# Performance work log

Hardware: AMD Instinct MI355X
Metric: run time of the kernel (lower is better)

## Reference

```python
import jax, jax.numpy as jnp
import numpy as np

B, N, D, K = 4, 4096, 64, 16
SCALE = float(np.sqrt(D))


def setup_inputs() -> dict:
    key = jax.random.key(0)
    ks = jax.random.split(key, 16)
    f = lambda i, shape: jax.random.normal(ks[i], shape, dtype=jnp.float32) * 0.05
    return {
        'x': jax.random.normal(ks[0], (B, N, D), dtype=jnp.float32),
        'pos': jax.random.uniform(ks[1], (B, N, 3), dtype=jnp.float32),
        'Wq': f(2, (D, D)), 'Wk': f(3, (D, D)), 'Wv': f(4, (D, D)),
        'P1': f(5, (3, D)), 'p1b': f(6, (D,)), 'P2': f(7, (D, D)), 'p2b': f(8, (D,)),
        'A1': f(9, (D, D)), 'a1b': f(10, (D,)), 'A2': f(11, (D, D)), 'a2b': f(12, (D,)),
        'Wf': f(13, (D, D)), 'bf': f(14, (D,)),
    }


def _gather(feats, idx):
    # feats: [B,N,C], idx: [B,N,K] -> [B,N,K,C]  (index_points / idx_pt)
    return jax.vmap(lambda f, i: f[i])(feats, idx)


def reference(x, pos, Wq, Wk, Wv, P1, p1b, P2, p2b, A1, a1b, A2, a2b, Wf, bf):
    # kNN via squared distances (same math as square_distance + argsort[:, :, :k])
    sq = jnp.sum(pos * pos, axis=-1)                                   # [B,N]
    dists = sq[:, :, None] + sq[:, None, :] - 2.0 * jnp.einsum('bnc,bmc->bnm', pos, pos)
    _, idx = jax.lax.top_k(-dists, K)                                  # [B,N,K]

    knn_xyz = _gather(pos, idx)                                        # [B,N,K,3]
    q = x @ Wq                                                         # [B,N,D]
    kf = _gather(x @ Wk, idx)                                          # [B,N,K,D]
    v = _gather(x @ Wv, idx)                                           # [B,N,K,D]

    rel = pos[:, :, None, :] - knn_xyz                                 # [B,N,K,3]
    pos_enc = jax.nn.relu(rel @ P1 + p1b) @ P2 + p2b                   # [B,N,K,D]

    attn = jax.nn.relu((q[:, :, None, :] - kf + pos_enc) @ A1 + a1b) @ A2 + a2b
    attn = jax.nn.softmax(attn / SCALE, axis=-2)                       # softmax over K

    agg = jnp.sum(attn * (v + pos_enc), axis=2)                        # [B,N,D]
    return agg @ Wf + bf + x                                           # residual
```

## Files before the change

kernel.cpp:

```cpp
#include <hip/hip_runtime.h>
#include <hip/hip_bf16.h>
#include <stdint.h>

#define B_ 4
#define N_ 4096
#define D_ 64
#define K_ 16

static const size_t OFS_WQA1  = 0;
static const size_t OFS_WKA1  = 4096;
static const size_t OFS_WCOMB = 8192;
static const size_t OFS_C1    = 16384;
static const size_t OFS_QA1   = 16448;
static const size_t OFS_KA1   = OFS_QA1 + (size_t)B_*N_*64;
static const size_t OFS_V     = OFS_KA1 + (size_t)B_*N_*64;
static const size_t OFS_IDX   = OFS_V   + (size_t)B_*N_*64;
static const size_t OFS_POS4  = OFS_IDX + (size_t)B_*N_*16;
static const size_t OFS_BF16  = OFS_POS4 + (size_t)B_*N_*4;
static const size_t OFS_PBF   = OFS_BF16 + 6144;
static const size_t OFS_WFB   = OFS_PBF + 6144;
static const size_t OFS_APK   = OFS_WFB + 2048;
static const size_t OFS_BPK   = OFS_APK + 262144;

#define KNN_CAP 96

typedef __attribute__((ext_vector_type(8))) short short8;
typedef __attribute__((ext_vector_type(4))) float floatx4;

__device__ __forceinline__ unsigned short f2bf(float f) {
    __hip_bfloat16 h = __float2bfloat16(f);
    return *reinterpret_cast<unsigned short*>(&h);
}

__device__ __forceinline__ float bf2f(unsigned short u) {
    __hip_bfloat16 h = *reinterpret_cast<__hip_bfloat16*>(&u);
    return __bfloat162float(h);
}

__device__ __forceinline__ unsigned long long bsortu64(unsigned long long v, int l) {
#pragma unroll
    for (int k = 2; k <= 64; k <<= 1) {
#pragma unroll
        for (int j = k >> 1; j > 0; j >>= 1) {
            unsigned long long o = __shfl_xor(v, j, 64);
            unsigned long long mn = v < o ? v : o;
            unsigned long long mx = v < o ? o : v;
            v = ((((l & j) == 0) == ((l & k) == 0))) ? mn : mx;
        }
    }
    return v;
}

__device__ __forceinline__ void bsortu64x2(unsigned long long& a, unsigned long long& b, int l) {
#pragma unroll
    for (int k = 2; k <= 64; k <<= 1) {
#pragma unroll
        for (int j = k >> 1; j > 0; j >>= 1) {
            unsigned long long oa = __shfl_xor(a, j, 64);
            unsigned long long ob = __shfl_xor(b, j, 64);
            bool up = (((l & j) == 0) == ((l & k) == 0));
            unsigned long long mna = a < oa ? a : oa, mxa = a < oa ? oa : a;
            unsigned long long mnb = b < ob ? b : ob, mxb = b < ob ? ob : b;
            a = up ? mna : mxa;
            b = up ? mnb : mxb;
        }
    }
}

__global__ __launch_bounds__(256) void k_pre(
        const float* __restrict__ Wq, const float* __restrict__ Wk,
        const float* __restrict__ Wv, const float* __restrict__ Wf,
        const float* __restrict__ P2, const float* __restrict__ A1,
        const float* __restrict__ p2b, const float* __restrict__ a1b,
        const float* __restrict__ pos, float* __restrict__ ws) {
    int blk = blockIdx.x;
    unsigned short* pbf = (unsigned short*)(ws + OFS_PBF);
    if (blk < 65) {
        int i = blk * 256 + threadIdx.x;
        if (i < 4096) {
            int c = i >> 6, d = i & 63;
            float s = 0.f;
            for (int e = 0; e < 64; ++e) s = fmaf(Wq[c*64+e], A1[e*64+d], s);
            ws[OFS_WQA1 + i] = s;
            pbf[d*64 + c] = f2bf(s);
        } else if (i < 8192) {
            int j = i - 4096; int c = j >> 6, d = j & 63;
            float s = 0.f;
            for (int e = 0; e < 64; ++e) s = fmaf(Wk[c*64+e], A1[e*64+d], s);
            ws[OFS_WKA1 + j] = s;
            pbf[(64+d)*64 + c] = f2bf(s);
        } else if (i < 16384) {
            int j = i - 8192; int c = j >> 7, dd = j & 127;
            float s;
            if (dd < 64) { s = 0.f; for (int e = 0; e < 64; ++e) s = fmaf(P2[c*64+e], A1[e*64+dd], s); }
            else s = P2[c*64 + (dd - 64)];
            ws[OFS_WCOMB + j] = s;
        } else if (i < 16448) {
            int d = i - 16384;
            float s = a1b[d];
            for (int e = 0; e < 64; ++e) s = fmaf(p2b[e], A1[e*64+d], s);
            ws[OFS_C1 + d] = s;
        }
    } else if (blk < 81) {
        int i = (blk - 65) * 256 + threadIdx.x;
        int c = i >> 6, d = i & 63;
        pbf[(128+d)*64 + c] = f2bf(Wv[c*64+d]);
    } else if (blk < 97) {
        int i = (blk - 81) * 256 + threadIdx.x;
        int c = i >> 6, d = i & 63;
        ((unsigned short*)(ws + OFS_WFB))[d*64 + c] = f2bf(Wf[c*64+d]);
    } else {
        int i = (blk - 97) * 256 + threadIdx.x;
        float px = pos[(size_t)i*3+0], py = pos[(size_t)i*3+1], pz = pos[(size_t)i*3+2];
        float sq = fmaf(pz, pz, fmaf(py, py, px*px));
        ((float4*)(ws + OFS_POS4))[i] = make_float4(px, py, pz, sq);

        unsigned short xh = f2bf(px), yh = f2bf(py), zh = f2bf(pz), sh = f2bf(sq);
        float xl = px - bf2f(xh), yl = py - bf2f(yh), zl = pz - bf2f(zh), sl = sq - bf2f(sh);
        unsigned short xlb = f2bf(xl), ylb = f2bf(yl), zlb = f2bf(zl), slb = f2bf(sl);
        unsigned short m2xh = f2bf(-2.f*bf2f(xh)), m2yh = f2bf(-2.f*bf2f(yh)), m2zh = f2bf(-2.f*bf2f(zh));
        unsigned short m2xl = f2bf(-2.f*xl), m2yl = f2bf(-2.f*yl), m2zl = f2bf(-2.f*zl);
        const unsigned short ONE = 0x3F80;
        union { unsigned short u[32]; uint4 v[4]; } A, Bp;
#pragma unroll
        for (int j2 = 0; j2 < 32; ++j2) { A.u[j2] = 0; Bp.u[j2] = 0; }
        A.u[0]=m2xh; A.u[1]=m2xh; A.u[2]=m2xl;
        A.u[3]=m2yh; A.u[4]=m2yh; A.u[5]=m2yl;
        A.u[6]=m2zh; A.u[7]=m2zh; A.u[8]=m2zl;
        A.u[9]=sh;   A.u[10]=slb; A.u[11]=ONE; A.u[12]=ONE;
        Bp.u[0]=xh;  Bp.u[1]=xlb; Bp.u[2]=xh;
        Bp.u[3]=yh;  Bp.u[4]=ylb; Bp.u[5]=yh;
        Bp.u[6]=zh;  Bp.u[7]=zlb; Bp.u[8]=zh;
        Bp.u[9]=ONE; Bp.u[10]=ONE; Bp.u[11]=sh; Bp.u[12]=slb;
        uint4* ap4 = (uint4*)(ws + OFS_APK);
        uint4* bp4 = (uint4*)(ws + OFS_BPK);
#pragma unroll
        for (int j2 = 0; j2 < 4; ++j2) { ap4[(size_t)i*4+j2] = A.v[j2]; bp4[(size_t)i*4+j2] = Bp.v[j2]; }
    }
}

__global__ __launch_bounds__(256) void k_projm(const float* __restrict__ x,
                                               const float* __restrict__ A2,
                                               float* __restrict__ ws) {
    __shared__ unsigned short xT[64*72];
    __shared__ unsigned short wTs[192*72];
    const int t = threadIdx.x;
    if (blockIdx.x >= 256) {
        int i = ((int)blockIdx.x - 256) * 256 + t;
        unsigned short* wbf = (unsigned short*)(ws + OFS_BF16);
        if (i < 8192) {
            int c = i >> 7, dd = i & 127;
            wbf[dd*64 + c] = f2bf(ws[OFS_WCOMB + i]);
        } else {
            int j = i - 8192; int e = j >> 6, d = j & 63;
            wbf[8192 + d*64 + e] = f2bf(A2[j]);
        }
        return;
    }
    const unsigned short* pbf = (const unsigned short*)(ws + OFS_PBF);
    const int g0 = (int)blockIdx.x * 64;

#pragma unroll
    for (int k = 0; k < 6; ++k) {
        int id  = t + 256*k;
        int row = id >> 3, cir = id & 7;
        uint4 vv = *(const uint4*)(pbf + row*64 + cir*8);
        *(uint4*)&wTs[row*72 + cir*8] = vv;
    }
    {
        int r = t >> 2, qd = t & 3;
        const float* src = x + (size_t)(g0 + r)*64 + qd*16;
        unsigned short hb[16];
#pragma unroll
        for (int u = 0; u < 16; ++u) hb[u] = f2bf(src[u]);
        *(uint4*)&xT[r*72 + qd*16]     = *(uint4*)&hb[0];
        *(uint4*)&xT[r*72 + qd*16 + 8] = *(uint4*)&hb[8];
    }
    __syncthreads();

    const int w = t >> 6, l = t & 63, lr = l & 15, q = l >> 4;
    floatx4 acc[12];
#pragma unroll
    for (int j = 0; j < 12; ++j) acc[j] = (floatx4){0.f, 0.f, 0.f, 0.f};
#pragma unroll
    for (int kb = 0; kb < 2; ++kb) {
        short8 a = *(const short8*)&xT[(16*w + lr)*72 + 32*kb + 8*q];
#pragma unroll
        for (int j = 0; j < 12; ++j) {
            short8 bfr = *(const short8*)&wTs[(16*j + lr)*72 + 32*kb + 8*q];
            acc[j] = __builtin_amdgcn_mfma_f32_16x16x32_bf16(a, bfr, acc[j], 0, 0, 0);
        }
    }
    float* qA1 = ws + OFS_QA1;
    float* kA1 = ws + OFS_KA1;
    float* vws = ws + OFS_V;
#pragma unroll
    for (int j = 0; j < 12; ++j) {
        int col = 16*j + lr;
        float* dst = (col < 64) ? qA1 : (col < 128 ? kA1 : vws);
        int c2 = col & 63;
#pragma unroll
        for (int r = 0; r < 4; ++r) {
            int grow = g0 + 16*w + 4*q + r;
            dst[(size_t)grow*64 + c2] = acc[j][r];
        }
    }
}

__device__ __forceinline__ unsigned long long knn_entry(
        const float4 q4, const float4* __restrict__ pos4b,
        const unsigned* __restrict__ s, int T, int e) {
    bool valid = e < T;
    int re = e < KNN_CAP ? e : KNN_CAP - 1;
    unsigned idxv = s[re];
    idxv = valid ? (idxv & 4095u) : 0u;
    float4 c4 = pos4b[idxv];
    float dot = fmaf(q4.z, c4.z, fmaf(q4.y, c4.y, q4.x*c4.x));
    float d = fmaxf(fmaf(-2.f, dot, q4.w + c4.w), 0.f);
    unsigned long long pk = ((unsigned long long)__float_as_uint(d) << 32) | idxv;
    return valid ? pk : ~0ull;
}

__device__ __forceinline__ unsigned long long knn_merge_rest1(
        unsigned long long best, int l, const float4 q4,
        const float4* __restrict__ pos4b, const unsigned* __restrict__ s, int T) {
    for (int base = 64; base < T; base += 64) {
        unsigned long long w2 = knn_entry(q4, pos4b, s, T, base + l);
        w2 = bsortu64(w2, l);
        unsigned long long bb = __shfl(w2, (l - 16) & 63, 64);
        unsigned long long nv = (l < 16) ? best : ((l < 32) ? bb : ~0ull);
        best = bsortu64(nv, l);
    }
    return best;
}

__global__ __launch_bounds__(512, 8) void k_knn(float* __restrict__ ws) {
    __shared__ float2 minbuf[16*16*9];
    __shared__ unsigned surv[16*KNN_CAP];
    __shared__ int   scnt[16];
    __shared__ float taubuf[16];
    const unsigned short* apk = (const unsigned short*)(ws + OFS_APK);
    const unsigned short* bpk = (const unsigned short*)(ws + OFS_BPK);
    const int t = threadIdx.x;
    const int w = t >> 6, l = t & 63;
    const int lr = l & 15, hi4 = l >> 4;
    const int g0 = (int)blockIdx.x * 16;
    const int b  = g0 >> 12;

    if (t < 16) scnt[t] = 0;

    short8 afrag = *(const short8*)(apk + (size_t)(g0 + lr)*32 + 8*hi4);
    const unsigned short* bbase = bpk + (size_t)(b*4096 + w*512 + lr)*32 + 8*hi4;
    const floatx4 z4 = {0.f, 0.f, 0.f, 0.f};

    float run1[4], run2[4];
#pragma unroll
    for (int r = 0; r < 4; ++r) { run1[r] = 1e30f; run2[r] = 1e30f; }
    {
        short8 cur[2], nxt[2];
#pragma unroll
        for (int u = 0; u < 2; ++u) cur[u] = *(const short8*)(bbase + u*512);
#pragma unroll 4
        for (int g = 0; g < 16; ++g) {
            const int gn = ((g + 1) & 15) * 2;
#pragma unroll
            for (int u = 0; u < 2; ++u) nxt[u] = *(const short8*)(bbase + (gn+u)*512);
#pragma unroll
            for (int u = 0; u < 2; ++u) {
                floatx4 a = __builtin_amdgcn_mfma_f32_16x16x32_bf16(afrag, cur[u], z4, 0, 0, 0);
#pragma unroll
                for (int r = 0; r < 4; ++r) {
                    run2[r] = fminf(run2[r], fmaxf(run1[r], a[r]));
                    run1[r] = fminf(run1[r], a[r]);
                }
            }
#pragma unroll
            for (int u = 0; u < 2; ++u) cur[u] = nxt[u];
        }
    }
#pragma unroll
    for (int r = 0; r < 4; ++r)
        minbuf[((4*hi4 + r)*16 + lr)*9 + w] = make_float2(run1[r], run2[r]);
    __syncthreads();

    if (t < 256) {
        int q = t >> 4, cl = t & 15;
        float m1 = 1e30f, m2 = 1e30f;
#pragma unroll
        for (int wv = 0; wv < 8; ++wv) {
            float2 p = minbuf[(q*16 + cl)*9 + wv];
            float hi = fmaxf(m1, p.x);
            m1 = fminf(m1, p.x);
            m2 = fminf(fminf(m2, p.y), hi);
        }
        float v = m2;
#pragma unroll
        for (int k = 2; k <= 16; k <<= 1) {
#pragma unroll
            for (int j = k >> 1; j > 0; j >>= 1) {
                float o = __shfl_xor(v, j, 64);
                bool up = (((cl & j) == 0) == ((cl & k) == 0));
                v = up ? fminf(v, o) : fmaxf(v, o);
            }
        }
        if (cl == 7) taubuf[q] = v + 1e-3f;
    }
    __syncthreads();

    float tau[4];
#pragma unroll
    for (int r = 0; r < 4; ++r) tau[r] = taubuf[4*hi4 + r];

    const unsigned cand0 = (unsigned)(w*512 + lr);
    {
        short8 cur[2], nxt[2];
#pragma unroll
        for (int u = 0; u < 2; ++u) cur[u] = *(const short8*)(bbase + u*512);
#pragma unroll 4
        for (int g = 0; g < 16; ++g) {
            const int gn = ((g + 1) & 15) * 2;
#pragma unroll
            for (int u = 0; u < 2; ++u) nxt[u] = *(const short8*)(bbase + (gn+u)*512);
#pragma unroll
            for (int u = 0; u < 2; ++u) {
                floatx4 a = __builtin_amdgcn_mfma_f32_16x16x32_bf16(afrag, cur[u], z4, 0, 0, 0);
                unsigned cid = cand0 + (unsigned)((g*2 + u)*16);
#pragma unroll
                for (int r = 0; r < 4; ++r) {
                    if (a[r] <= tau[r]) {
                        int p = atomicAdd(&scnt[4*hi4 + r], 1);
                        if (p < KNN_CAP) surv[(4*hi4 + r)*KNN_CAP + p] = cid;
                    }
                }
            }
#pragma unroll
            for (int u = 0; u < 2; ++u) cur[u] = nxt[u];
        }
    }
    __syncthreads();

    const float4* pos4g = (const float4*)(ws + OFS_POS4);
    const float4* pos4b = pos4g + (size_t)b * N_;
    int* idx = (int*)(ws + OFS_IDX);
    int qa = 2*w, qb = 2*w + 1;
    int Ta = scnt[qa]; Ta = Ta < KNN_CAP ? Ta : KNN_CAP;
    int Tb = scnt[qb]; Tb = Tb < KNN_CAP ? Tb : KNN_CAP;
    const unsigned* sa = surv + qa*KNN_CAP;
    const unsigned* sb = surv + qb*KNN_CAP;
    float4 q4a = pos4g[g0 + qa];
    float4 q4b = pos4g[g0 + qb];
    unsigned long long pk0 = knn_entry(q4a, pos4b, sa, Ta, l);
    unsigned long long pk1 = knn_entry(q4b, pos4b, sb, Tb, l);
    bsortu64x2(pk0, pk1, l);
    if (Ta > 64) pk0 = knn_merge_rest1(pk0, l, q4a, pos4b, sa, Ta);
    if (Tb > 64) pk1 = knn_merge_rest1(pk1, l, q4b, pos4b, sb, Tb);
    if (l < 16) {
        idx[(size_t)(g0 + qa)*16 + l] = (int)(pk0 & 0xFFFu);
        idx[(size_t)(g0 + qb)*16 + l] = (int)(pk1 & 0xFFFu);
    }
}

__global__ __launch_bounds__(256) void k_attn(
    const float* __restrict__ x, const float* __restrict__ pos,
    const float* __restrict__ P1, const float* __restrict__ p1b,
    const float* __restrict__ p2b, const float* __restrict__ a2b,
    const float* __restrict__ bff, const float* __restrict__ ws,
    float* __restrict__ out) {

    __shared__ unsigned short wT[128*72];
    __shared__ unsigned short a2T[64*72];
    __shared__ unsigned short abuf[128*72];
    __shared__ float relb[128*4];
    __shared__ int   mrow[128];

    const int t  = threadIdx.x;
    const int g0 = blockIdx.x * 8;
    const int b  = g0 >> 12;
    const float* qA1 = ws + OFS_QA1;
    const float* kA1 = ws + OFS_KA1;
    const float* vws = ws + OFS_V;
    const float* c1  = ws + OFS_C1;
    const int* idx = (const int*)(ws + OFS_IDX);
    const unsigned short* wbf = (const unsigned short*)(ws + OFS_BF16);
    const unsigned short* wfb = (const unsigned short*)(ws + OFS_WFB);

#pragma unroll
    for (int k = 0; k < 6; ++k) {
        int id  = t + 256*k;
        int row = id >> 3, cir = id & 7;
        uint4 vv = *(const uint4*)(wbf + row*64 + cir*8);
        if (row < 128) *(uint4*)&wT[row*72 + cir*8] = vv;
        else           *(uint4*)&a2T[(row-128)*72 + cir*8] = vv;
    }

    if (t < 128) {
        int p = t >> 4, k = t & 15;
        int ng = g0 + p;
        int m  = idx[(size_t)ng*16 + k];
        int mg = b * N_ + m;
        mrow[t] = mg;
        relb[t*4+0] = pos[(size_t)ng*3+0] - pos[(size_t)mg*3+0];
        relb[t*4+1] = pos[(size_t)ng*3+1] - pos[(size_t)mg*3+1];
        relb[t*4+2] = pos[(size_t)ng*3+2] - pos[(size_t)mg*3+2];
    }
    __syncthreads();

    const int w = t >> 6, l = t & 63, lr = l & 15, q = l >> 4;

    float kpre[2][4][4];
    float qpre[2][4];
#pragma unroll
    for (int i = 0; i < 2; ++i) {
        int ng = g0 + 2*w + i;
#pragma unroll
        for (int j = 0; j < 4; ++j) {
            int col = 16*j + lr;
            qpre[i][j] = qA1[(size_t)ng*64 + col] + c1[col];
#pragma unroll
            for (int r = 0; r < 4; ++r) {
                int row = 32*w + 16*i + 4*q + r;
                kpre[i][j][r] = kA1[(size_t)mrow[row]*64 + col];
            }
        }
    }

    {
        int d = t & 63, r0 = t >> 6;
        float w0 = P1[d], w1 = P1[64+d], w2 = P1[128+d], bb = p1b[d];
#pragma unroll
        for (int jj = 0; jj < 32; ++jj) {
            int r = r0 + jj*4;
            float h = fmaf(relb[r*4+2], w2, fmaf(relb[r*4+1], w1, fmaf(relb[r*4+0], w0, bb)));
            abuf[r*72 + d] = f2bf(fmaxf(h, 0.f));
        }
    }
    __syncthreads();

    floatx4 acc1[2][8];
#pragma unroll
    for (int i = 0; i < 2; ++i)
#pragma unroll
        for (int j = 0; j < 8; ++j) acc1[i][j] = (floatx4){0.f, 0.f, 0.f, 0.f};
#pragma unroll
    for (int kb = 0; kb < 2; ++kb) {
        short8 a0 = *(const short8*)&abuf[(32*w      + lr)*72 + 32*kb + 8*q];
        short8 a1 = *(const short8*)&abuf[(32*w + 16 + lr)*72 + 32*kb + 8*q];
#pragma unroll
        for (int j = 0; j < 8; ++j) {
            short8 bfr = *(const short8*)&wT[(16*j + lr)*72 + 32*kb + 8*q];
            acc1[0][j] = __builtin_amdgcn_mfma_f32_16x16x32_bf16(a0, bfr, acc1[0][j], 0, 0, 0);
            acc1[1][j] = __builtin_amdgcn_mfma_f32_16x16x32_bf16(a1, bfr, acc1[1][j], 0, 0, 0);
        }
    }
    __syncthreads();

#pragma unroll
    for (int i = 0; i < 2; ++i) {
#pragma unroll
        for (int j = 0; j < 4; ++j) {
            int col = 16*j + lr;
            float qv = qpre[i][j];
#pragma unroll
            for (int r = 0; r < 4; ++r) {
                int row = 32*w + 16*i + 4*q + r;
                float t1 = acc1[i][j][r] + qv - kpre[i][j][r];
                abuf[row*72 + col] = f2bf(fmaxf(t1, 0.f));
            }
        }
    }

    float vpre[2][4][4];
#pragma unroll
    for (int i = 0; i < 2; ++i)
#pragma unroll
        for (int j = 0; j < 4; ++j) {
            int col = 16*j + lr;
#pragma unroll
            for (int r = 0; r < 4; ++r) {
                int row = 32*w + 16*i + 4*q + r;
                vpre[i][j][r] = vws[(size_t)mrow[row]*64 + col];
            }
        }
    short8 wffrag[2];
#pragma unroll
    for (int kb = 0; kb < 2; ++kb)
        wffrag[kb] = *(const short8*)&wfb[(16*w + lr)*64 + 32*kb + 8*q];
    __syncthreads();

    floatx4 acc2[2][4];
#pragma unroll
    for (int i = 0; i < 2; ++i)
#pragma unroll
        for (int j = 0; j < 4; ++j) acc2[i][j] = (floatx4){0.f, 0.f, 0.f, 0.f};
#pragma unroll
    for (int kb = 0; kb < 2; ++kb) {
        short8 a0 = *(const short8*)&abuf[(32*w      + lr)*72 + 32*kb + 8*q];
        short8 a1 = *(const short8*)&abuf[(32*w + 16 + lr)*72 + 32*kb + 8*q];
#pragma unroll
        for (int j = 0; j < 4; ++j) {
            short8 bfr = *(const short8*)&a2T[(16*j + lr)*72 + 32*kb + 8*q];
            acc2[0][j] = __builtin_amdgcn_mfma_f32_16x16x32_bf16(a0, bfr, acc2[0][j], 0, 0, 0);
            acc2[1][j] = __builtin_amdgcn_mfma_f32_16x16x32_bf16(a1, bfr, acc2[1][j], 0, 0, 0);
        }
    }
    __syncthreads();

#pragma unroll
    for (int i = 0; i < 2; ++i) {
#pragma unroll
        for (int j = 0; j < 4; ++j) {
            int col = 16*j + lr;
            float a2bv = a2b[col], p2bv = p2b[col];
            float L[4];
#pragma unroll
            for (int r = 0; r < 4; ++r) L[r] = acc2[i][j][r] + a2bv;
            float mx = fmaxf(fmaxf(L[0], L[1]), fmaxf(L[2], L[3]));
            mx = fmaxf(mx, __shfl_xor(mx, 16, 64));
            mx = fmaxf(mx, __shfl_xor(mx, 32, 64));
            float ssum = 0.f, part = 0.f;
#pragma unroll
            for (int r = 0; r < 4; ++r) {
                float e = __expf((L[r] - mx) * 0.125f);
                ssum += e;
                float wv = vpre[i][j][r] + (acc1[i][4+j][r] + p2bv);
                part = fmaf(e, wv, part);
            }
            ssum += __shfl_xor(ssum, 16, 64);
            ssum += __shfl_xor(ssum, 32, 64);
            part += __shfl_xor(part, 16, 64);
            part += __shfl_xor(part, 32, 64);
            float agg = part / ssum;
            if (q == 0) abuf[(2*w + i)*72 + col] = f2bf(agg);
        }
    }
    __syncthreads();

    {
        floatx4 accF = (floatx4){0.f, 0.f, 0.f, 0.f};
#pragma unroll
        for (int kb = 0; kb < 2; ++kb) {
            short8 afr = *(const short8*)&abuf[lr*72 + 32*kb + 8*q];
            accF = __builtin_amdgcn_mfma_f32_16x16x32_bf16(afr, wffrag[kb], accF, 0, 0, 0);
        }
        if (q < 2) {
            int col = 16*w + lr;
            float bv = bff[col];
#pragma unroll
            for (int r = 0; r < 4; ++r) {
                int g = g0 + 4*q + r;
                out[(size_t)g*64 + col] = accF[r] + bv + x[(size_t)g*64 + col];
            }
        }
    }
}

extern "C" void kernel_launch(void* const* d_in, const int* in_sizes, int n_in,
                              void* d_out, int out_size, void* d_ws, size_t ws_size,
                              hipStream_t stream) {
    const float* x   = (const float*)d_in[0];
    const float* pos = (const float*)d_in[1];
    const float* Wq  = (const float*)d_in[2];
    const float* Wk  = (const float*)d_in[3];
    const float* Wv  = (const float*)d_in[4];
    const float* P1  = (const float*)d_in[5];
    const float* p1b = (const float*)d_in[6];
    const float* P2  = (const float*)d_in[7];
    const float* p2b = (const float*)d_in[8];
    const float* A1  = (const float*)d_in[9];
    const float* a1b = (const float*)d_in[10];
    const float* A2  = (const float*)d_in[11];
    const float* a2b = (const float*)d_in[12];
    const float* Wf  = (const float*)d_in[13];
    const float* bf  = (const float*)d_in[14];
    float* out = (float*)d_out;
    float* ws  = (float*)d_ws;

    hipLaunchKernelGGL(k_pre,   dim3(161),  dim3(256), 0, stream,
                       Wq, Wk, Wv, Wf, P2, A1, p2b, a1b, pos, ws);
    hipLaunchKernelGGL(k_projm, dim3(304),  dim3(256), 0, stream, x, A2, ws);
    hipLaunchKernelGGL(k_knn,   dim3(1024), dim3(512), 0, stream, ws);
    hipLaunchKernelGGL(k_attn,  dim3(2048), dim3(256), 0, stream,
                       x, pos, P1, p1b, p2b, a2b, bf, ws, out);
}
```

Measured before the change: 170.7 us.

## Merge projection kernel into kNN launch as extra blocks and reorder candidate scan

Folds the k_projm projection/bf16-conversion work into the k_knn launch as additional block ranges sharing one aliased shared-memory buffer, removing one kernel launch and letting projection blocks overlap with kNN blocks. The projection is re-split across 512 threads (two wave groups each taking half of the output column tiles). The kNN scan loops are restructured to process two candidate groups 16 tiles apart per iteration with full unrolling, and launch bounds drop occupancy hint from 8 to 4 blocks. Risks include lower occupancy hints, higher register pressure from full unrolling, and changed candidate order in the atomic survivor list.

```diff
diff --git a/kernel.cpp b/kernel.cpp
--- a/kernel.cpp
+++ b/kernel.cpp
@@ -139,74 +139,6 @@
     }
 }
 
-__global__ __launch_bounds__(256) void k_projm(const float* __restrict__ x,
-                                               const float* __restrict__ A2,
-                                               float* __restrict__ ws) {
-    __shared__ unsigned short xT[64*72];
-    __shared__ unsigned short wTs[192*72];
-    const int t = threadIdx.x;
-    if (blockIdx.x >= 256) {
-        int i = ((int)blockIdx.x - 256) * 256 + t;
-        unsigned short* wbf = (unsigned short*)(ws + OFS_BF16);
-        if (i < 8192) {
-            int c = i >> 7, dd = i & 127;
-            wbf[dd*64 + c] = f2bf(ws[OFS_WCOMB + i]);
-        } else {
-            int j = i - 8192; int e = j >> 6, d = j & 63;
-            wbf[8192 + d*64 + e] = f2bf(A2[j]);
-        }
-        return;
-    }
-    const unsigned short* pbf = (const unsigned short*)(ws + OFS_PBF);
-    const int g0 = (int)blockIdx.x * 64;
-
-#pragma unroll
-    for (int k = 0; k < 6; ++k) {
-        int id  = t + 256*k;
-        int row = id >> 3, cir = id & 7;
-        uint4 vv = *(const uint4*)(pbf + row*64 + cir*8);
-        *(uint4*)&wTs[row*72 + cir*8] = vv;
-    }
-    {
-        int r = t >> 2, qd = t & 3;
-        const float* src = x + (size_t)(g0 + r)*64 + qd*16;
-        unsigned short hb[16];
-#pragma unroll
-        for (int u = 0; u < 16; ++u) hb[u] = f2bf(src[u]);
-        *(uint4*)&xT[r*72 + qd*16]     = *(uint4*)&hb[0];
-        *(uint4*)&xT[r*72 + qd*16 + 8] = *(uint4*)&hb[8];
-    }
-    __syncthreads();
-
-    const int w = t >> 6, l = t & 63, lr = l & 15, q = l >> 4;
-    floatx4 acc[12];
-#pragma unroll
-    for (int j = 0; j < 12; ++j) acc[j] = (floatx4){0.f, 0.f, 0.f, 0.f};
-#pragma unroll
-    for (int kb = 0; kb < 2; ++kb) {
-        short8 a = *(const short8*)&xT[(16*w + lr)*72 + 32*kb + 8*q];
-#pragma unroll
-        for (int j = 0; j < 12; ++j) {
-            short8 bfr = *(const short8*)&wTs[(16*j + lr)*72 + 32*kb + 8*q];
-            acc[j] = __builtin_amdgcn_mfma_f32_16x16x32_bf16(a, bfr, acc[j], 0, 0, 0);
-        }
-    }
-    float* qA1 = ws + OFS_QA1;
-    float* kA1 = ws + OFS_KA1;
-    float* vws = ws + OFS_V;
-#pragma unroll
-    for (int j = 0; j < 12; ++j) {
-        int col = 16*j + lr;
-        float* dst = (col < 64) ? qA1 : (col < 128 ? kA1 : vws);
-        int c2 = col & 63;
-#pragma unroll
-        for (int r = 0; r < 4; ++r) {
-            int grow = g0 + 16*w + 4*q + r;
-            dst[(size_t)grow*64 + c2] = acc[j][r];
-        }
-    }
-}
-
 __device__ __forceinline__ unsigned long long knn_entry(
         const float4 q4, const float4* __restrict__ pos4b,
         const unsigned* __restrict__ s, int T, int e) {
@@ -234,17 +166,89 @@
     return best;
 }
 
-__global__ __launch_bounds__(512, 8) void k_knn(float* __restrict__ ws) {
-    __shared__ float2 minbuf[16*16*9];
-    __shared__ unsigned surv[16*KNN_CAP];
-    __shared__ int   scnt[16];
-    __shared__ float taubuf[16];
+__global__ __launch_bounds__(512, 4) void k_knn(const float* __restrict__ x,
+                                                const float* __restrict__ A2,
+                                                float* __restrict__ ws) {
+    __shared__ __align__(16) unsigned char smem[36864];
+    const int bid = (int)blockIdx.x;
+    const int t = threadIdx.x;
+
+    if (bid >= 1024) {
+        if (bid >= 1280) {
+            int i = (bid - 1280) * 512 + t;
+            unsigned short* wbf = (unsigned short*)(ws + OFS_BF16);
+            if (i < 8192) {
+                int c = i >> 7, dd = i & 127;
+                wbf[dd*64 + c] = f2bf(ws[OFS_WCOMB + i]);
+            } else {
+                int j = i - 8192; int e = j >> 6, d = j & 63;
+                wbf[8192 + d*64 + e] = f2bf(A2[j]);
+            }
+            return;
+        }
+        unsigned short* xT  = (unsigned short*)smem;
+        unsigned short* wTs = (unsigned short*)(smem + 9216);
+        const unsigned short* pbf = (const unsigned short*)(ws + OFS_PBF);
+        const int g0 = (bid - 1024) * 64;
+
+#pragma unroll
+        for (int k = 0; k < 3; ++k) {
+            int id  = t + 512*k;
+            int row = id >> 3, cir = id & 7;
+            uint4 vv = *(const uint4*)(pbf + row*64 + cir*8);
+            *(uint4*)&wTs[row*72 + cir*8] = vv;
+        }
+        {
+            int r = t >> 3, qd = t & 7;
+            const float* src = x + (size_t)(g0 + r)*64 + qd*8;
+            unsigned short hb[8];
+#pragma unroll
+            for (int u = 0; u < 8; ++u) hb[u] = f2bf(src[u]);
+            *(uint4*)&xT[r*72 + qd*8] = *(uint4*)&hb[0];
+        }
+        __syncthreads();
+
+        const int w = t >> 6, l = t & 63, lr = l & 15, q = l >> 4;
+        const int w4 = w & 3, jh = w >> 2;
+        floatx4 acc[6];
+#pragma unroll
+        for (int j = 0; j < 6; ++j) acc[j] = (floatx4){0.f, 0.f, 0.f, 0.f};
+#pragma unroll
+        for (int kb = 0; kb < 2; ++kb) {
+            short8 a = *(const short8*)&xT[(16*w4 + lr)*72 + 32*kb + 8*q];
+#pragma unroll
+            for (int j = 0; j < 6; ++j) {
+                int jj = jh*6 + j;
+                short8 bfr = *(const short8*)&wTs[(16*jj + lr)*72 + 32*kb + 8*q];
+                acc[j] = __builtin_amdgcn_mfma_f32_16x16x32_bf16(a, bfr, acc[j], 0, 0, 0);
+            }
+        }
+        float* qA1 = ws + OFS_QA1;
+        float* kA1 = ws + OFS_KA1;
+        float* vws = ws + OFS_V;
+#pragma unroll
+        for (int j = 0; j < 6; ++j) {
+            int col = 16*(jh*6 + j) + lr;
+            float* dst = (col < 64) ? qA1 : (col < 128 ? kA1 : vws);
+            int c2 = col & 63;
+#pragma unroll
+            for (int r = 0; r < 4; ++r) {
+                int grow = g0 + 16*w4 + 4*q + r;
+                dst[(size_t)grow*64 + c2] = acc[j][r];
+            }
+        }
+        return;
+    }
+
+    float2* minbuf   = (float2*)smem;
+    unsigned* surv   = (unsigned*)(smem + 18432);
+    int* scnt        = (int*)(smem + 18432 + 6144);
+    float* taubuf    = (float*)(smem + 18432 + 6144 + 64);
     const unsigned short* apk = (const unsigned short*)(ws + OFS_APK);
     const unsigned short* bpk = (const unsigned short*)(ws + OFS_BPK);
-    const int t = threadIdx.x;
     const int w = t >> 6, l = t & 63;
     const int lr = l & 15, hi4 = l >> 4;
-    const int g0 = (int)blockIdx.x * 16;
+    const int g0 = bid * 16;
     const int b  = g0 >> 12;
 
     if (t < 16) scnt[t] = 0;
@@ -257,25 +261,23 @@
 #pragma unroll
     for (int r = 0; r < 4; ++r) { run1[r] = 1e30f; run2[r] = 1e30f; }
     {
-        short8 cur[2], nxt[2];
-#pragma unroll
-        for (int u = 0; u < 2; ++u) cur[u] = *(const short8*)(bbase + u*512);
-#pragma unroll 4
+        short8 cA = *(const short8*)(bbase);
+        short8 cB = *(const short8*)(bbase + 16*512);
+#pragma unroll
         for (int g = 0; g < 16; ++g) {
-            const int gn = ((g + 1) & 15) * 2;
-#pragma unroll
-            for (int u = 0; u < 2; ++u) nxt[u] = *(const short8*)(bbase + (gn+u)*512);
-#pragma unroll
-            for (int u = 0; u < 2; ++u) {
-                floatx4 a = __builtin_amdgcn_mfma_f32_16x16x32_bf16(afrag, cur[u], z4, 0, 0, 0);
-#pragma unroll
-                for (int r = 0; r < 4; ++r) {
-                    run2[r] = fminf(run2[r], fmaxf(run1[r], a[r]));
-                    run1[r] = fminf(run1[r], a[r]);
-                }
-            }
-#pragma unroll
-            for (int u = 0; u < 2; ++u) cur[u] = nxt[u];
+            const int gn = (g + 1) & 15;
+            short8 nA = *(const short8*)(bbase + gn*512);
+            short8 nB = *(const short8*)(bbase + (16+gn)*512);
+            floatx4 aA = __builtin_amdgcn_mfma_f32_16x16x32_bf16(afrag, cA, z4, 0, 0, 0);
+            floatx4 aB = __builtin_amdgcn_mfma_f32_16x16x32_bf16(afrag, cB, z4, 0, 0, 0);
+#pragma unroll
+            for (int r = 0; r < 4; ++r) {
+                run2[r] = fminf(run2[r], fmaxf(run1[r], aA[r]));
+                run1[r] = fminf(run1[r], aA[r]);
+                run2[r] = fminf(run2[r], fmaxf(run1[r], aB[r]));
+                run1[r] = fminf(run1[r], aB[r]);
+            }
+            cA = nA; cB = nB;
         }
     }
 #pragma unroll
@@ -312,29 +314,31 @@
     for (int r = 0; r < 4; ++r) tau[r] = taubuf[4*hi4 + r];
 
     const unsigned cand0 = (unsigned)(w*512 + lr);
+    const int qb0 = 4*hi4;
     {
-        short8 cur[2], nxt[2];
-#pragma unroll
-        for (int u = 0; u < 2; ++u) cur[u] = *(const short8*)(bbase + u*512);
-#pragma unroll 4
+        short8 cA = *(const short8*)(bbase);
+        short8 cB = *(const short8*)(bbase + 16*512);
+#pragma unroll
         for (int g = 0; g < 16; ++g) {
-            const int gn = ((g + 1) & 15) * 2;
-#pragma unroll
-            for (int u = 0; u < 2; ++u) nxt[u] = *(const short8*)(bbase + (gn+u)*512);
-#pragma unroll
-            for (int u = 0; u < 2; ++u) {
-                floatx4 a = __builtin_amdgcn_mfma_f32_16x16x32_bf16(afrag, cur[u], z4, 0, 0, 0);
-                unsigned cid = cand0 + (unsigned)((g*2 + u)*16);
-#pragma unroll
-                for (int r = 0; r < 4; ++r) {
-                    if (a[r] <= tau[r]) {
-                        int p = atomicAdd(&scnt[4*hi4 + r], 1);
-                        if (p < KNN_CAP) surv[(4*hi4 + r)*KNN_CAP + p] = cid;
-                    }
+            const int gn = (g + 1) & 15;
+            short8 nA = *(const short8*)(bbase + gn*512);
+            short8 nB = *(const short8*)(bbase + (16+gn)*512);
+            floatx4 aA = __builtin_amdgcn_mfma_f32_16x16x32_bf16(afrag, cA, z4, 0, 0, 0);
+            floatx4 aB = __builtin_amdgcn_mfma_f32_16x16x32_bf16(afrag, cB, z4, 0, 0, 0);
+            unsigned cidA = cand0 + (unsigned)(g*16);
+            unsigned cidB = cand0 + (unsigned)((16+g)*16);
+#pragma unroll
+            for (int r = 0; r < 4; ++r) {
+                if (aA[r] <= tau[r]) {
+                    int p = atomicAdd(&scnt[qb0+r], 1);
+                    if (p < KNN_CAP) surv[(qb0+r)*KNN_CAP + p] = cidA;
                 }
-            }
-#pragma unroll
-            for (int u = 0; u < 2; ++u) cur[u] = nxt[u];
+                if (aB[r] <= tau[r]) {
+                    int p = atomicAdd(&scnt[qb0+r], 1);
+                    if (p < KNN_CAP) surv[(qb0+r)*KNN_CAP + p] = cidB;
+                }
+            }
+            cA = nA; cB = nB;
         }
     }
     __syncthreads();
@@ -577,8 +581,7 @@
 
     hipLaunchKernelGGL(k_pre,   dim3(161),  dim3(256), 0, stream,
                        Wq, Wk, Wv, Wf, P2, A1, p2b, a1b, pos, ws);
-    hipLaunchKernelGGL(k_projm, dim3(304),  dim3(256), 0, stream, x, A2, ws);
-    hipLaunchKernelGGL(k_knn,   dim3(1024), dim3(512), 0, stream, ws);
+    hipLaunchKernelGGL(k_knn,   dim3(1304), dim3(512), 0, stream, x, A2, ws);
     hipLaunchKernelGGL(k_attn,  dim3(2048), dim3(256), 0, stream,
                        x, pos, P1, p1b, p2b, a2b, bf, ws, out);
 }
```

After: 164.5 us. -3.6%, faster.
